# Optimization experiments

Measured on AMD Instinct MI355X. Metric: run time of the kernel, lower is better.

Reference implementation:

```python
import jax, jax.numpy as jnp
import numpy as np

N_NODES = 100000
N_EDGES = 1600000
INPUT_DIM = 512
HIDDEN = 64
N_LAYERS = 3


def setup_inputs() -> dict:
    key = jax.random.key(0)
    ks = jax.random.split(key, 8)
    s = 0.05
    return {
        "x": jax.random.normal(ks[0], (N_NODES, INPUT_DIM), jnp.float32),
        "edge_index": jax.random.randint(ks[1], (2, N_EDGES), 0, N_NODES, jnp.int64),
        "W_enc": jax.random.normal(ks[2], (INPUT_DIM, HIDDEN), jnp.float32) * s,
        "b_enc": jnp.zeros((HIDDEN,), jnp.float32),
        "Wl": jax.random.normal(ks[3], (N_LAYERS, HIDDEN, HIDDEN), jnp.float32) * s,
        "bl": jnp.zeros((N_LAYERS, HIDDEN), jnp.float32),
        "Wr": jax.random.normal(ks[4], (N_LAYERS, HIDDEN, HIDDEN), jnp.float32) * s,
        "W_cls": jax.random.normal(ks[5], (HIDDEN, 1), jnp.float32) * s,
        "b_cls": jnp.zeros((1,), jnp.float32),
    }


def reference(x, edge_index, W_enc, b_enc, Wl, bl, Wr, W_cls, b_cls):
    # node encoder
    h = x @ W_enc + b_enc  # [N, H]
    N = h.shape[0]
    src, dst = edge_index[0], edge_index[1]  # messages flow src -> dst (PyG convention)
    ones = jnp.ones((src.shape[0],), h.dtype)
    deg = jax.ops.segment_sum(ones, dst, num_segments=N)  # in-degree per node
    inv_deg = jnp.where(deg > 0, 1.0 / jnp.maximum(deg, 1.0), 0.0)[:, None]
    n_layers = Wl.shape[0]
    for l in range(n_layers):
        # SAGEConv: mean-aggregate neighbor features, transform, add root transform
        msgs = h[src]  # [E, H] gather
        agg = jax.ops.segment_sum(msgs, dst, num_segments=N) * inv_deg  # mean aggr
        h_new = agg @ Wl[l] + bl[l] + h @ Wr[l]
        h = jax.nn.relu(h + h_new)  # residual + relu
    out = jax.nn.sigmoid(h @ W_cls + b_cls)  # [N, 1]
    return out.squeeze(-1)
```

## Files before the change

### kernel.cpp

```cpp
#include <hip/hip_runtime.h>
#include <math.h>

#define HID 64
#define KIN 512

typedef __attribute__((ext_vector_type(8))) short short8;
typedef __attribute__((ext_vector_type(4))) float floatx4;

__device__ inline unsigned bf16pair(float a, float b) {
  unsigned ua = __float_as_uint(a);
  unsigned ub = __float_as_uint(b);
  ua = (ua + 0x7FFFu + ((ua >> 16) & 1u)) >> 16;
  ub = (ub + 0x7FFFu + ((ub >> 16) & 1u)) >> 16;
  return ua | (ub << 16);
}
__device__ inline unsigned short bf16one(float a) {
  unsigned ua = __float_as_uint(a);
  return (unsigned short)((ua + 0x7FFFu + ((ua >> 16) & 1u)) >> 16);
}
__device__ inline unsigned char fp8q(float a) {
  const int pk = __builtin_amdgcn_cvt_pk_fp8_f32(a, a, 0, false);
  return (unsigned char)(pk & 0xff);
}

__global__ __launch_bounds__(256) void prep_hist_kernel(
    const float* __restrict__ We, const float* __restrict__ Wl,
    const float* __restrict__ Wr, unsigned short* __restrict__ wte,
    unsigned short* __restrict__ wlrt, const int* __restrict__ dst,
    int* __restrict__ cnt, int* __restrict__ rank, int E, int N) {
  const int blk = blockIdx.x;
  const int tid = threadIdx.x;
  if (blk < 128) {
    const int t = blk * 256 + tid;
    const int c = t >> 9, k = t & 511;
    wte[c * KIN + k] = bf16one(We[k * HID + c]);
  } else if (blk < 224) {
    const int t = (blk - 128) * 256 + tid;
    const int mat = t >> 12;
    const int e = t & 4095;
    const int c = e >> 6, k = e & 63;
    const float* src =
        (mat < 3) ? (Wl + (size_t)mat * 4096) : (Wr + (size_t)(mat - 3) * 4096);
    wlrt[(size_t)mat * 4096 + c * 64 + k] = bf16one(src[k * 64 + c]);
  } else {
    const int e = (blk - 224) * 256 + tid;
    if (e < E) {
      const int d = dst[e];
      if ((unsigned)d < (unsigned)N) rank[e] = atomicAdd(&cnt[d], 1);
    }
  }
}

__global__ __launch_bounds__(1024) void scanA_kernel(
    const int* __restrict__ cnt, int* __restrict__ block_sums, int N) {
  __shared__ int red[1024];
  const int tid = threadIdx.x;
  const int i = blockIdx.x * 1024 + tid;
  red[tid] = (i < N) ? cnt[i] : 0;
  __syncthreads();
  for (int off = 512; off > 0; off >>= 1) {
    if (tid < off) red[tid] += red[tid + off];
    __syncthreads();
  }
  if (tid == 0) block_sums[blockIdx.x] = red[0];
}

__global__ __launch_bounds__(1024) void scanC_kernel(
    const int* __restrict__ cnt, const int* __restrict__ block_sums,
    int* __restrict__ row_start, float* __restrict__ inv_deg, int N) {
  __shared__ int part[1024];
  __shared__ int soff;
  const int tid = threadIdx.x;
  const int i = blockIdx.x * 1024 + tid;
  if (tid < 64) {
    int s = 0;
    for (int b2 = tid; b2 < blockIdx.x; b2 += 64) s += block_sums[b2];
#pragma unroll
    for (int off = 32; off > 0; off >>= 1) s += __shfl_down(s, off, 64);
    if (tid == 0) soff = s;
  }
  const int v = (i < N) ? cnt[i] : 0;
  part[tid] = v;
  __syncthreads();
  for (int off = 1; off < 1024; off <<= 1) {
    int t = (tid >= off) ? part[tid - off] : 0;
    __syncthreads();
    part[tid] += t;
    __syncthreads();
  }
  if (i < N) {
    row_start[i] = soff + part[tid] - v;
    inv_deg[i] = (v > 0) ? 1.0f / (float)v : 0.0f;
  }
  if (blockIdx.x == gridDim.x - 1 && tid == 1023)
    row_start[N] = soff + part[1023];
}

__global__ __launch_bounds__(256) void scatter_enc_kernel(
    const int* __restrict__ src, const int* __restrict__ dst,
    const int* __restrict__ row_start, const int* __restrict__ rank,
    int* __restrict__ csr_src, const float* __restrict__ x,
    const unsigned short* __restrict__ wt, const float* __restrict__ b,
    unsigned short* __restrict__ hb, unsigned char* __restrict__ h8, int E,
    int N) {
  __shared__ uint4 sx[2][256];
  __shared__ uint4 sw[2][256];
  const int nscat = (E + 255) >> 8;
  if (blockIdx.x < nscat) {
    const int e = blockIdx.x * 256 + threadIdx.x;
    if (e < E) {
      const int d = dst[e];
      if ((unsigned)d < (unsigned)N) {
        int s = src[e];
        if ((unsigned)s >= (unsigned)N) s = 0;
        csr_src[row_start[d] + rank[e]] = s;
      }
    }
    return;
  }
  const int t = threadIdx.x;
  const int lane = t & 63;
  const int wid = t >> 6;
  const int m15 = lane & 15;
  const int quad = lane >> 4;
  const int blockBase = (blockIdx.x - nscat) * 64;

  const int rs = t >> 2;
  const int qs = t & 3;
  const int us = rs * 4 + (qs ^ ((rs >> 1) & 3));
  const int gn = blockBase + rs;
  const bool valid = gn < N;
  const float* xp = x + (size_t)(valid ? gn : 0) * KIN + qs * 8;
  const unsigned short* wp = wt + (size_t)rs * KIN + qs * 8;

  const int arow = wid * 16 + m15;
  const int ua = arow * 4 + (quad ^ ((arow >> 1) & 3));
  int ub[4];
#pragma unroll
  for (int c4 = 0; c4 < 4; c4++) {
    const int col = c4 * 16 + m15;
    ub[c4] = col * 4 + (quad ^ ((col >> 1) & 3));
  }

  floatx4 acc[4];
#pragma unroll
  for (int c4 = 0; c4 < 4; c4++)
#pragma unroll
    for (int j = 0; j < 4; j++) acc[c4][j] = 0.f;

  float4 fx0, fx1;
  uint4 wv;
  if (valid) {
    fx0 = *(const float4*)(xp);
    fx1 = *(const float4*)(xp + 4);
  } else {
    fx0 = fx1 = make_float4(0.f, 0.f, 0.f, 0.f);
  }
  wv = *(const uint4*)(wp);

  for (int kc = 0; kc < 16; kc++) {
    const int cur = kc & 1;
    uint4 xu;
    xu.x = bf16pair(fx0.x, fx0.y);
    xu.y = bf16pair(fx0.z, fx0.w);
    xu.z = bf16pair(fx1.x, fx1.y);
    xu.w = bf16pair(fx1.z, fx1.w);
    sx[cur][us] = xu;
    sw[cur][us] = wv;
    __syncthreads();
    if (kc < 15) {
      const int ko = (kc + 1) * 32;
      if (valid) {
        fx0 = *(const float4*)(xp + ko);
        fx1 = *(const float4*)(xp + ko + 4);
      }
      wv = *(const uint4*)(wp + ko);
    }
    const short8 a = __builtin_bit_cast(short8, sx[cur][ua]);
#pragma unroll
    for (int c4 = 0; c4 < 4; c4++) {
      const short8 bf = __builtin_bit_cast(short8, sw[cur][ub[c4]]);
      acc[c4] =
          __builtin_amdgcn_mfma_f32_16x16x32_bf16(a, bf, acc[c4], 0, 0, 0);
    }
  }

#pragma unroll
  for (int c4 = 0; c4 < 4; c4++) {
    const float bias = b[c4 * 16 + m15];
#pragma unroll
    for (int r = 0; r < 4; r++) {
      const int row = blockBase + wid * 16 + quad * 4 + r;
      if (row < N) {
        const float v = acc[c4][r] + bias;
        hb[(size_t)row * HID + c4 * 16 + m15] = bf16one(v);
        h8[(size_t)row * HID + c4 * 16 + m15] = fp8q(v);
      }
    }
  }
}

__global__ __launch_bounds__(256) void layer_kernel(
    const unsigned short* __restrict__ hin,
    const unsigned char* __restrict__ h8in, unsigned short* __restrict__ hout,
    unsigned char* __restrict__ h8out, const int* __restrict__ row_start,
    const int* __restrict__ csr_src, const float* __restrict__ inv_deg,
    const unsigned short* __restrict__ Wlt,
    const unsigned short* __restrict__ Wrt, const float* __restrict__ bl,
    const float* __restrict__ Wc, const float* __restrict__ bc,
    float* __restrict__ out, int N) {
  __shared__ uint4 sAgg[512];
  __shared__ uint4 sH[512];
  __shared__ uint4 sWl[512];
  __shared__ uint4 sWr[512];
  const int tid = threadIdx.x;
  const int lane = tid & 63;
  const int wid = tid >> 6;
  const int m15 = lane & 15;
  const int quad = lane >> 4;
  const int blockBase = blockIdx.x * 64;

  {
    const int r = tid >> 2;
    const int gp = tid & 3;
    const int g0 = gp * 2, g1 = gp * 2 + 1;
    const int u0 = r * 8 + (g0 ^ (r & 7));
    const int u1 = r * 8 + (g1 ^ (r & 7));
    const int gn = blockBase + r;
    if (gn < N) {
      const uint4* hp = (const uint4*)(hin + (size_t)gn * HID);
      sH[u0] = hp[g0];
      sH[u1] = hp[g1];
    } else {
      const uint4 z = make_uint4(0, 0, 0, 0);
      sH[u0] = z;
      sH[u1] = z;
    }
    const uint4* wl = (const uint4*)(Wlt + (size_t)r * HID);
    const uint4* wr = (const uint4*)(Wrt + (size_t)r * HID);
    sWl[u0] = wl[g0];
    sWl[u1] = wl[g1];
    sWr[u0] = wr[g0];
    sWr[u1] = wr[g1];
  }

  {
    const int slot = lane >> 2;
    const int qc = lane & 3;
    const int nl = wid * 16 + slot;
    const int gn = blockBase + nl;
    float a[16];
#pragma unroll
    for (int c = 0; c < 16; c++) a[c] = 0.f;
    float id = 0.f;
    if (gn < N) {
      id = inv_deg[gn];
      const int s = row_start[gn];
      const int e = row_start[gn + 1];
      for (int j = s; j < e; j += 8) {
        int n[8];
        bool ok[8];
#pragma unroll
        for (int u = 0; u < 8; u++) {
          const int jj = j + u;
          ok[u] = jj < e;
          n[u] = csr_src[ok[u] ? jj : j];
        }
        uint4 v[8];
#pragma unroll
        for (int u = 0; u < 8; u++) {
          v[u] = *(const uint4*)(h8in + (size_t)n[u] * HID + qc * 16);
        }
#pragma unroll
        for (int u = 0; u < 8; u++) {
          if (!ok[u]) v[u] = make_uint4(0, 0, 0, 0);
          a[0] += __builtin_amdgcn_cvt_f32_fp8(v[u].x, 0);
          a[1] += __builtin_amdgcn_cvt_f32_fp8(v[u].x, 1);
          a[2] += __builtin_amdgcn_cvt_f32_fp8(v[u].x, 2);
          a[3] += __builtin_amdgcn_cvt_f32_fp8(v[u].x, 3);
          a[4] += __builtin_amdgcn_cvt_f32_fp8(v[u].y, 0);
          a[5] += __builtin_amdgcn_cvt_f32_fp8(v[u].y, 1);
          a[6] += __builtin_amdgcn_cvt_f32_fp8(v[u].y, 2);
          a[7] += __builtin_amdgcn_cvt_f32_fp8(v[u].y, 3);
          a[8] += __builtin_amdgcn_cvt_f32_fp8(v[u].z, 0);
          a[9] += __builtin_amdgcn_cvt_f32_fp8(v[u].z, 1);
          a[10] += __builtin_amdgcn_cvt_f32_fp8(v[u].z, 2);
          a[11] += __builtin_amdgcn_cvt_f32_fp8(v[u].z, 3);
          a[12] += __builtin_amdgcn_cvt_f32_fp8(v[u].w, 0);
          a[13] += __builtin_amdgcn_cvt_f32_fp8(v[u].w, 1);
          a[14] += __builtin_amdgcn_cvt_f32_fp8(v[u].w, 2);
          a[15] += __builtin_amdgcn_cvt_f32_fp8(v[u].w, 3);
        }
      }
    }
    uint4 p0, p1;
    p0.x = bf16pair(a[0] * id, a[1] * id);
    p0.y = bf16pair(a[2] * id, a[3] * id);
    p0.z = bf16pair(a[4] * id, a[5] * id);
    p0.w = bf16pair(a[6] * id, a[7] * id);
    p1.x = bf16pair(a[8] * id, a[9] * id);
    p1.y = bf16pair(a[10] * id, a[11] * id);
    p1.z = bf16pair(a[12] * id, a[13] * id);
    p1.w = bf16pair(a[14] * id, a[15] * id);
    sAgg[nl * 8 + ((qc * 2) ^ (nl & 7))] = p0;
    sAgg[nl * 8 + ((qc * 2 + 1) ^ (nl & 7))] = p1;
  }
  __syncthreads();

  floatx4 acc[4];
#pragma unroll
  for (int c4 = 0; c4 < 4; c4++)
#pragma unroll
    for (int j = 0; j < 4; j++) acc[c4][j] = 0.f;

  const int arow = wid * 16 + m15;
#pragma unroll
  for (int c = 0; c < 2; c++) {
    const int ua = arow * 8 + ((c * 4 + quad) ^ (arow & 7));
    const short8 aA = __builtin_bit_cast(short8, sAgg[ua]);
    const short8 aH = __builtin_bit_cast(short8, sH[ua]);
#pragma unroll
    for (int c4 = 0; c4 < 4; c4++) {
      const int col = c4 * 16 + m15;
      const int ub = col * 8 + ((c * 4 + quad) ^ (col & 7));
      acc[c4] = __builtin_amdgcn_mfma_f32_16x16x32_bf16(
          aA, __builtin_bit_cast(short8, sWl[ub]), acc[c4], 0, 0, 0);
      acc[c4] = __builtin_amdgcn_mfma_f32_16x16x32_bf16(
          aH, __builtin_bit_cast(short8, sWr[ub]), acc[c4], 0, 0, 0);
    }
  }

  float vals[4][4];
#pragma unroll
  for (int c4 = 0; c4 < 4; c4++) {
    const float bias = bl[c4 * 16 + m15];
#pragma unroll
    for (int r = 0; r < 4; r++) {
      const int rowl = wid * 16 + quad * 4 + r;
      const unsigned short hv =
          ((const unsigned short*)
               sH)[(rowl * 8 + ((c4 * 2 + (m15 >> 3)) ^ (rowl & 7))) * 8 +
                   (m15 & 7)];
      const float v = __uint_as_float((unsigned)hv << 16) + acc[c4][r] + bias;
      vals[c4][r] = v > 0.f ? v : 0.f;
    }
  }
#pragma unroll
  for (int c4 = 0; c4 < 4; c4++) {
#pragma unroll
    for (int r = 0; r < 4; r++) {
      const int rowg = blockBase + wid * 16 + quad * 4 + r;
      if (rowg < N)
        hout[(size_t)rowg * HID + c4 * 16 + m15] = bf16one(vals[c4][r]);
    }
  }
  if (h8out != nullptr) {
#pragma unroll
    for (int c4 = 0; c4 < 4; c4++) {
#pragma unroll
      for (int r = 0; r < 4; r++) {
        const int rowg = blockBase + wid * 16 + quad * 4 + r;
        if (rowg < N)
          h8out[(size_t)rowg * HID + c4 * 16 + m15] = fp8q(vals[c4][r]);
      }
    }
  }
  if (Wc != nullptr) {
    float p[4] = {0.f, 0.f, 0.f, 0.f};
#pragma unroll
    for (int c4 = 0; c4 < 4; c4++) {
      const float wc = Wc[c4 * 16 + m15];
#pragma unroll
      for (int r = 0; r < 4; r++) p[r] += vals[c4][r] * wc;
    }
#pragma unroll
    for (int off = 1; off < 16; off <<= 1) {
#pragma unroll
      for (int r = 0; r < 4; r++) p[r] += __shfl_xor(p[r], off, 16);
    }
    if (m15 == 0) {
      const float bb = bc[0];
#pragma unroll
      for (int r = 0; r < 4; r++) {
        const int rowg = blockBase + wid * 16 + quad * 4 + r;
        if (rowg < N) out[rowg] = 1.0f / (1.0f + expf(-(p[r] + bb)));
      }
    }
  }
}

extern "C" void kernel_launch(void* const* d_in, const int* in_sizes, int n_in,
                              void* d_out, int out_size, void* d_ws,
                              size_t ws_size, hipStream_t stream) {
  const float* x = (const float*)d_in[0];
  const int* ei = (const int*)d_in[1];
  const float* W_enc = (const float*)d_in[2];
  const float* b_enc = (const float*)d_in[3];
  const float* Wl = (const float*)d_in[4];
  const float* bl = (const float*)d_in[5];
  const float* Wr = (const float*)d_in[6];
  const float* Wc = (const float*)d_in[7];
  const float* bc = (const float*)d_in[8];
  float* out = (float*)d_out;

  const int N = in_sizes[0] / KIN;
  const int E = in_sizes[1] / 2;
  const int* src = ei;
  const int* dst = ei + E;

  char* ws = (char*)d_ws;
  size_t off = 0;
  auto alloc = [&](size_t bytes) -> void* {
    void* p = ws + off;
    off += (bytes + 255) & ~(size_t)255;
    return p;
  };
  unsigned short* hb0 =
      (unsigned short*)alloc((size_t)N * HID * sizeof(unsigned short));
  unsigned short* hb1 =
      (unsigned short*)alloc((size_t)N * HID * sizeof(unsigned short));
  unsigned char* h8a = (unsigned char*)alloc((size_t)N * HID);
  unsigned char* h8b = (unsigned char*)alloc((size_t)N * HID);
  int* cnt = (int*)alloc((size_t)N * sizeof(int));
  int* rank = (int*)alloc((size_t)E * sizeof(int));
  int* row_start = (int*)alloc((size_t)(N + 1) * sizeof(int));
  float* inv_deg = (float*)alloc((size_t)N * sizeof(float));
  int* csr_src = (int*)alloc((size_t)E * sizeof(int));
  const int nblk = (N + 1023) / 1024;
  int* block_sums = (int*)alloc((size_t)nblk * sizeof(int));
  unsigned short* wte =
      (unsigned short*)alloc((size_t)HID * KIN * sizeof(unsigned short));
  unsigned short* wlrt =
      (unsigned short*)alloc((size_t)6 * HID * HID * sizeof(unsigned short));

  hipMemsetAsync(cnt, 0, (size_t)N * sizeof(int), stream);

  const int nhist = (E + 255) / 256;
  prep_hist_kernel<<<224 + nhist, 256, 0, stream>>>(W_enc, Wl, Wr, wte, wlrt,
                                                    dst, cnt, rank, E, N);
  scanA_kernel<<<nblk, 1024, 0, stream>>>(cnt, block_sums, N);
  scanC_kernel<<<nblk, 1024, 0, stream>>>(cnt, block_sums, row_start, inv_deg,
                                          N);
  const int nscat = (E + 255) / 256;
  const int nb64 = (N + 63) / 64;
  scatter_enc_kernel<<<nscat + nb64, 256, 0, stream>>>(
      src, dst, row_start, rank, csr_src, x, wte, b_enc, hb0, h8a, E, N);

  layer_kernel<<<nb64, 256, 0, stream>>>(hb0, h8a, hb1, h8b, row_start, csr_src,
                                         inv_deg, wlrt, wlrt + 3 * 4096, bl,
                                         nullptr, nullptr, nullptr, N);
  layer_kernel<<<nb64, 256, 0, stream>>>(hb1, h8b, hb0, h8a, row_start, csr_src,
                                         inv_deg, wlrt + 4096, wlrt + 4 * 4096,
                                         bl + 64, nullptr, nullptr, nullptr, N);
  layer_kernel<<<nb64, 256, 0, stream>>>(hb0, h8a, hb1, nullptr, row_start,
                                         csr_src, inv_deg, wlrt + 2 * 4096,
                                         wlrt + 5 * 4096, bl + 128, Wc, bc, out,
                                         N);
}
```

Before: 513.1 us.

## Build CSR via destination-bucketed edge buffers and read layer weights from global

```diff
diff --git a/kernel.cpp b/kernel.cpp
--- a/kernel.cpp
+++ b/kernel.cpp
@@ -3,9 +3,11 @@
 
 #define HID 64
 #define KIN 512
+#define NBK_MAX 256
 
 typedef __attribute__((ext_vector_type(8))) short short8;
 typedef __attribute__((ext_vector_type(4))) float floatx4;
+typedef __attribute__((ext_vector_type(2))) float floatx2;
 
 __device__ inline unsigned bf16pair(float a, float b) {
   unsigned ua = __float_as_uint(a);
@@ -23,30 +25,77 @@
   return (unsigned char)(pk & 0xff);
 }
 
-__global__ __launch_bounds__(256) void prep_hist_kernel(
+__global__ __launch_bounds__(1024) void prep_hist_bucket_kernel(
     const float* __restrict__ We, const float* __restrict__ Wl,
     const float* __restrict__ Wr, unsigned short* __restrict__ wte,
-    unsigned short* __restrict__ wlrt, const int* __restrict__ dst,
-    int* __restrict__ cnt, int* __restrict__ rank, int E, int N) {
+    unsigned short* __restrict__ wlrt, const int* __restrict__ src,
+    const int* __restrict__ dst, int* __restrict__ cnt,
+    int* __restrict__ gcur, unsigned* __restrict__ ebuf, int E, int N,
+    int nhist, int NBK, int CAP) {
   const int blk = blockIdx.x;
   const int tid = threadIdx.x;
-  if (blk < 128) {
-    const int t = blk * 256 + tid;
+  if (blk < 32) {
+    const int t = blk * 1024 + tid;
     const int c = t >> 9, k = t & 511;
     wte[c * KIN + k] = bf16one(We[k * HID + c]);
-  } else if (blk < 224) {
-    const int t = (blk - 128) * 256 + tid;
-    const int mat = t >> 12;
-    const int e = t & 4095;
-    const int c = e >> 6, k = e & 63;
-    const float* src =
-        (mat < 3) ? (Wl + (size_t)mat * 4096) : (Wr + (size_t)(mat - 3) * 4096);
-    wlrt[(size_t)mat * 4096 + c * 64 + k] = bf16one(src[k * 64 + c]);
-  } else {
-    const int e = (blk - 224) * 256 + tid;
+    return;
+  }
+  if (blk < 56) {
+    const int t = (blk - 32) * 1024 + tid;
+    if (t < 24576) {
+      const int mat = t >> 12;
+      const int e = t & 4095;
+      const int c = e >> 6, k = e & 63;
+      const float* sp = (mat < 3) ? (Wl + (size_t)mat * 4096)
+                                  : (Wr + (size_t)(mat - 3) * 4096);
+      wlrt[(size_t)mat * 4096 + c * 64 + k] = bf16one(sp[k * 64 + c]);
+    }
+    return;
+  }
+  if (blk < 56 + nhist) {
+    const int e = (blk - 56) * 1024 + tid;
     if (e < E) {
       const int d = dst[e];
-      if ((unsigned)d < (unsigned)N) rank[e] = atomicAdd(&cnt[d], 1);
+      if ((unsigned)d < (unsigned)N) atomicAdd(&cnt[d], 1);
+    }
+    return;
+  }
+  __shared__ int hist[NBK_MAX];
+  __shared__ int bbase[NBK_MAX];
+  __shared__ int curloc[NBK_MAX];
+  const int e0 = (blk - 56 - nhist) * 4096;
+  for (int i = tid; i < NBK; i += 1024) {
+    hist[i] = 0;
+    curloc[i] = 0;
+  }
+  __syncthreads();
+  int bk[4];
+  unsigned pk[4];
+#pragma unroll
+  for (int u = 0; u < 4; u++) {
+    const int e = e0 + u * 1024 + tid;
+    bk[u] = -1;
+    pk[u] = 0;
+    if (e < E) {
+      const int d = dst[e];
+      if ((unsigned)d < (unsigned)N) {
+        int s = src[e];
+        if ((unsigned)s >= (unsigned)N) s = 0;
+        bk[u] = d >> 9;
+        pk[u] = ((unsigned)s << 9) | (unsigned)(d & 511);
+        atomicAdd(&hist[bk[u]], 1);
+      }
+    }
+  }
+  __syncthreads();
+  for (int i = tid; i < NBK; i += 1024)
+    if (hist[i]) bbase[i] = atomicAdd(&gcur[i], hist[i]);
+  __syncthreads();
+#pragma unroll
+  for (int u = 0; u < 4; u++) {
+    if (bk[u] >= 0) {
+      const int gp = bbase[bk[u]] + atomicAdd(&curloc[bk[u]], 1);
+      if (gp < CAP) ebuf[(size_t)bk[u] * CAP + gp] = pk[u];
     }
   }
 }
@@ -97,24 +146,33 @@
 }
 
 __global__ __launch_bounds__(256) void scatter_enc_kernel(
-    const int* __restrict__ src, const int* __restrict__ dst,
-    const int* __restrict__ row_start, const int* __restrict__ rank,
-    int* __restrict__ csr_src, const float* __restrict__ x,
-    const unsigned short* __restrict__ wt, const float* __restrict__ b,
-    unsigned short* __restrict__ hb, unsigned char* __restrict__ h8, int E,
-    int N) {
+    const unsigned* __restrict__ ebuf, const int* __restrict__ gcur,
+    const int* __restrict__ row_start, int* __restrict__ csr_src,
+    const float* __restrict__ x, const unsigned short* __restrict__ wt,
+    const float* __restrict__ b, unsigned short* __restrict__ hb,
+    unsigned char* __restrict__ h8, int N, int NBK, int CAP) {
   __shared__ uint4 sx[2][256];
   __shared__ uint4 sw[2][256];
-  const int nscat = (E + 255) >> 8;
-  if (blockIdx.x < nscat) {
-    const int e = blockIdx.x * 256 + threadIdx.x;
-    if (e < E) {
-      const int d = dst[e];
-      if ((unsigned)d < (unsigned)N) {
-        int s = src[e];
-        if ((unsigned)s >= (unsigned)N) s = 0;
-        csr_src[row_start[d] + rank[e]] = s;
-      }
+  __shared__ int cur[512];
+  __shared__ int rsl[512];
+  if (blockIdx.x < (unsigned)NBK) {
+    const int bkt = blockIdx.x;
+    const int nodeBase = bkt << 9;
+    const int tid = threadIdx.x;
+    cur[tid] = 0;
+    cur[tid + 256] = 0;
+    rsl[tid] = (nodeBase + tid < N) ? row_start[nodeBase + tid] : 0;
+    rsl[tid + 256] =
+        (nodeBase + tid + 256 < N) ? row_start[nodeBase + tid + 256] : 0;
+    __syncthreads();
+    int cnt_b = gcur[bkt];
+    if (cnt_b > CAP) cnt_b = CAP;
+    const unsigned* eb = ebuf + (size_t)bkt * CAP;
+    for (int i = tid; i < cnt_b; i += 256) {
+      const unsigned p = eb[i];
+      const int dl = p & 511;
+      const int pos = rsl[dl] + atomicAdd(&cur[dl], 1);
+      csr_src[pos] = (int)(p >> 9);
     }
     return;
   }
@@ -123,7 +181,7 @@
   const int wid = t >> 6;
   const int m15 = lane & 15;
   const int quad = lane >> 4;
-  const int blockBase = (blockIdx.x - nscat) * 64;
+  const int blockBase = (blockIdx.x - NBK) * 64;
 
   const int rs = t >> 2;
   const int qs = t & 3;
@@ -159,14 +217,14 @@
   wv = *(const uint4*)(wp);
 
   for (int kc = 0; kc < 16; kc++) {
-    const int cur = kc & 1;
+    const int curb = kc & 1;
     uint4 xu;
     xu.x = bf16pair(fx0.x, fx0.y);
     xu.y = bf16pair(fx0.z, fx0.w);
     xu.z = bf16pair(fx1.x, fx1.y);
     xu.w = bf16pair(fx1.z, fx1.w);
-    sx[cur][us] = xu;
-    sw[cur][us] = wv;
+    sx[curb][us] = xu;
+    sw[curb][us] = wv;
     __syncthreads();
     if (kc < 15) {
       const int ko = (kc + 1) * 32;
@@ -176,10 +234,10 @@
       }
       wv = *(const uint4*)(wp + ko);
     }
-    const short8 a = __builtin_bit_cast(short8, sx[cur][ua]);
+    const short8 a = __builtin_bit_cast(short8, sx[curb][ua]);
 #pragma unroll
     for (int c4 = 0; c4 < 4; c4++) {
-      const short8 bf = __builtin_bit_cast(short8, sw[cur][ub[c4]]);
+      const short8 bf = __builtin_bit_cast(short8, sw[curb][ub[c4]]);
       acc[c4] =
           __builtin_amdgcn_mfma_f32_16x16x32_bf16(a, bf, acc[c4], 0, 0, 0);
     }
@@ -211,8 +269,6 @@
     float* __restrict__ out, int N) {
   __shared__ uint4 sAgg[512];
   __shared__ uint4 sH[512];
-  __shared__ uint4 sWl[512];
-  __shared__ uint4 sWr[512];
   const int tid = threadIdx.x;
   const int lane = tid & 63;
   const int wid = tid >> 6;
@@ -236,12 +292,6 @@
       sH[u0] = z;
       sH[u1] = z;
     }
-    const uint4* wl = (const uint4*)(Wlt + (size_t)r * HID);
-    const uint4* wr = (const uint4*)(Wrt + (size_t)r * HID);
-    sWl[u0] = wl[g0];
-    sWl[u1] = wl[g1];
-    sWr[u0] = wr[g0];
-    sWr[u1] = wr[g1];
   }
 
   {
@@ -274,6 +324,27 @@
 #pragma unroll
         for (int u = 0; u < 8; u++) {
           if (!ok[u]) v[u] = make_uint4(0, 0, 0, 0);
+#if __has_builtin(__builtin_amdgcn_cvt_pk_f32_fp8)
+          {
+            floatx2 p;
+            p = __builtin_amdgcn_cvt_pk_f32_fp8((int)v[u].x, false);
+            a[0] += p[0]; a[1] += p[1];
+            p = __builtin_amdgcn_cvt_pk_f32_fp8((int)v[u].x, true);
+            a[2] += p[0]; a[3] += p[1];
+            p = __builtin_amdgcn_cvt_pk_f32_fp8((int)v[u].y, false);
+            a[4] += p[0]; a[5] += p[1];
+            p = __builtin_amdgcn_cvt_pk_f32_fp8((int)v[u].y, true);
+            a[6] += p[0]; a[7] += p[1];
+            p = __builtin_amdgcn_cvt_pk_f32_fp8((int)v[u].z, false);
+            a[8] += p[0]; a[9] += p[1];
+            p = __builtin_amdgcn_cvt_pk_f32_fp8((int)v[u].z, true);
+            a[10] += p[0]; a[11] += p[1];
+            p = __builtin_amdgcn_cvt_pk_f32_fp8((int)v[u].w, false);
+            a[12] += p[0]; a[13] += p[1];
+            p = __builtin_amdgcn_cvt_pk_f32_fp8((int)v[u].w, true);
+            a[14] += p[0]; a[15] += p[1];
+          }
+#else
           a[0] += __builtin_amdgcn_cvt_f32_fp8(v[u].x, 0);
           a[1] += __builtin_amdgcn_cvt_f32_fp8(v[u].x, 1);
           a[2] += __builtin_amdgcn_cvt_f32_fp8(v[u].x, 2);
@@ -290,6 +361,7 @@
           a[13] += __builtin_amdgcn_cvt_f32_fp8(v[u].w, 1);
           a[14] += __builtin_amdgcn_cvt_f32_fp8(v[u].w, 2);
           a[15] += __builtin_amdgcn_cvt_f32_fp8(v[u].w, 3);
+#endif
         }
       }
     }
@@ -322,11 +394,14 @@
 #pragma unroll
     for (int c4 = 0; c4 < 4; c4++) {
       const int col = c4 * 16 + m15;
-      const int ub = col * 8 + ((c * 4 + quad) ^ (col & 7));
+      const uint4 wlv =
+          *(const uint4*)(Wlt + (size_t)col * HID + (c * 4 + quad) * 8);
+      const uint4 wrv =
+          *(const uint4*)(Wrt + (size_t)col * HID + (c * 4 + quad) * 8);
       acc[c4] = __builtin_amdgcn_mfma_f32_16x16x32_bf16(
-          aA, __builtin_bit_cast(short8, sWl[ub]), acc[c4], 0, 0, 0);
+          aA, __builtin_bit_cast(short8, wlv), acc[c4], 0, 0, 0);
       acc[c4] = __builtin_amdgcn_mfma_f32_16x16x32_bf16(
-          aH, __builtin_bit_cast(short8, sWr[ub]), acc[c4], 0, 0, 0);
+          aH, __builtin_bit_cast(short8, wrv), acc[c4], 0, 0, 0);
     }
   }
 
@@ -407,6 +482,11 @@
   const int E = in_sizes[1] / 2;
   const int* src = ei;
   const int* dst = ei + E;
+
+  const int NBK = (N + 511) >> 9;
+  int CAP = E / (NBK > 0 ? NBK : 1);
+  CAP = CAP + (CAP >> 1) + 1024;
+  CAP = (CAP + 255) & ~255;
 
   char* ws = (char*)d_ws;
   size_t off = 0;
@@ -422,10 +502,11 @@
   unsigned char* h8a = (unsigned char*)alloc((size_t)N * HID);
   unsigned char* h8b = (unsigned char*)alloc((size_t)N * HID);
   int* cnt = (int*)alloc((size_t)N * sizeof(int));
-  int* rank = (int*)alloc((size_t)E * sizeof(int));
+  int* gcur = (int*)alloc((size_t)NBK * sizeof(int));
   int* row_start = (int*)alloc((size_t)(N + 1) * sizeof(int));
   float* inv_deg = (float*)alloc((size_t)N * sizeof(float));
   int* csr_src = (int*)alloc((size_t)E * sizeof(int));
+  unsigned* ebuf = (unsigned*)alloc((size_t)NBK * CAP * sizeof(unsigned));
   const int nblk = (N + 1023) / 1024;
   int* block_sums = (int*)alloc((size_t)nblk * sizeof(int));
   unsigned short* wte =
@@ -434,17 +515,19 @@
       (unsigned short*)alloc((size_t)6 * HID * HID * sizeof(unsigned short));
 
   hipMemsetAsync(cnt, 0, (size_t)N * sizeof(int), stream);
-
-  const int nhist = (E + 255) / 256;
-  prep_hist_kernel<<<224 + nhist, 256, 0, stream>>>(W_enc, Wl, Wr, wte, wlrt,
-                                                    dst, cnt, rank, E, N);
+  hipMemsetAsync(gcur, 0, (size_t)NBK * sizeof(int), stream);
+
+  const int nhist = (E + 1023) / 1024;
+  const int nbktA = (E + 4095) / 4096;
+  prep_hist_bucket_kernel<<<56 + nhist + nbktA, 1024, 0, stream>>>(
+      W_enc, Wl, Wr, wte, wlrt, src, dst, cnt, gcur, ebuf, E, N, nhist, NBK,
+      CAP);
   scanA_kernel<<<nblk, 1024, 0, stream>>>(cnt, block_sums, N);
   scanC_kernel<<<nblk, 1024, 0, stream>>>(cnt, block_sums, row_start, inv_deg,
                                           N);
-  const int nscat = (E + 255) / 256;
   const int nb64 = (N + 63) / 64;
-  scatter_enc_kernel<<<nscat + nb64, 256, 0, stream>>>(
-      src, dst, row_start, rank, csr_src, x, wte, b_enc, hb0, h8a, E, N);
+  scatter_enc_kernel<<<NBK + nb64, 256, 0, stream>>>(
+      ebuf, gcur, row_start, csr_src, x, wte, b_enc, hb0, h8a, N, NBK, CAP);
 
   layer_kernel<<<nb64, 256, 0, stream>>>(hb0, h8a, hb1, h8b, row_start, csr_src,
                                          inv_deg, wlrt, wlrt + 3 * 4096, bl,
```

Measured after the change: 516.7 us. No clear change (+0.7%).
